# Optimization experiments

Hardware: AMD Instinct MI355X
Metric: run time of the kernel (lower is better)

Reference implementation:

```python
import jax, jax.numpy as jnp
import numpy as np

EPS_LN = 1e-5

def _ln(x, w, b):
    m = x.mean(-1, keepdims=True)
    v = x.var(-1, keepdims=True)  # biased var, matching torch LayerNorm
    return (x - m) / jnp.sqrt(v + EPS_LN) * w + b


def setup_inputs() -> dict:
    key = jax.random.key(0)
    ks = jax.random.split(key, 20)
    B, N, C = 8, 4096, 256
    def lin_w(k, i, o):
        return (jax.random.normal(k, (i, o), jnp.float32) / np.sqrt(i)).astype(jnp.float32)
    inp = {
        'xyz': jax.random.normal(ks[0], (B, N, 3), jnp.float32),
        'features': jax.random.normal(ks[1], (B, N, C), jnp.float32),
        # geo_mlp: Linear(10,32), LN(32), ReLU, Linear(32,16)
        'g_w1': lin_w(ks[2], 10, 32), 'g_b1': jnp.zeros((32,), jnp.float32),
        'g_lnw': jnp.ones((32,), jnp.float32), 'g_lnb': jnp.zeros((32,), jnp.float32),
        'g_w2': lin_w(ks[3], 32, 16), 'g_b2': jnp.zeros((16,), jnp.float32),
        # edge_pred: Linear(C+16,64), LN(64), ReLU, Linear(64,1), Sigmoid
        'e_w1': lin_w(ks[4], C + 16, 64), 'e_b1': jnp.zeros((64,), jnp.float32),
        'e_lnw': jnp.ones((64,), jnp.float32), 'e_lnb': jnp.zeros((64,), jnp.float32),
        'e_w2': lin_w(ks[5], 64, 1), 'e_b2': jnp.zeros((1,), jnp.float32),
        # edge_refine: Linear(C,C), LN(C), ReLU
        'r_w': lin_w(ks[6], C, C), 'r_b': jnp.zeros((C,), jnp.float32),
        'r_lnw': jnp.ones((C,), jnp.float32), 'r_lnb': jnp.zeros((C,), jnp.float32),
    }
    return inp


def reference(xyz, features, g_w1, g_b1, g_lnw, g_lnb, g_w2, g_b2,
              e_w1, e_b1, e_lnw, e_lnb, e_w2, e_b2, r_w, r_b, r_lnw, r_lnb):
    k = 16
    # KNN: pairwise negative squared distance, top-k largest = nearest
    sq = jnp.sum(xyz * xyz, axis=-1)                              # [B,N]
    pd = 2.0 * jnp.einsum('bnd,bmd->bnm', xyz, xyz) - sq[:, :, None] - sq[:, None, :]
    idx = jax.lax.top_k(pd, k)[1]                                 # [B,N,k]
    nbr = jax.vmap(lambda p, i: p[i])(xyz, idx)                   # [B,N,k,3]
    cen = nbr - nbr.mean(axis=2, keepdims=True)                   # centered neighborhoods
    cov = jnp.einsum('bnkc,bnkd->bncd', cen, cen) / k             # [B,N,3,3]
    trace = cov[..., 0, 0] + cov[..., 1, 1] + cov[..., 2, 2]
    det = jnp.clip(cov[..., 0, 0] * cov[..., 1, 1] * cov[..., 2, 2], 1e-8, None)
    std = jnp.std(cen, axis=2, ddof=1)                            # [B,N,3] (torch unbiased std)
    d = jnp.linalg.norm(cen, axis=3)                              # [B,N,k]
    mean_d = d.mean(axis=2)
    std_d = jnp.std(d, axis=2, ddof=1)
    t = trace + 1e-6
    geo = jnp.stack([trace, det, std[..., 0], std[..., 1], std[..., 2],
                     mean_d, std_d, std[..., 0] / t, std[..., 1] / t, std[..., 2] / t], axis=-1)
    geo = jax.nn.relu(_ln(geo @ g_w1 + g_b1, g_lnw, g_lnb)) @ g_w2 + g_b2    # [B,N,16]
    comb = jnp.concatenate([features, geo], axis=-1)
    edge_prob = jax.nn.sigmoid(jax.nn.relu(_ln(comb @ e_w1 + e_b1, e_lnw, e_lnb)) @ e_w2 + e_b2)
    refined = jax.nn.relu(_ln(features @ r_w + r_b, r_lnw, r_lnb))
    refined = features + refined * edge_prob
    return refined, edge_prob
```

## Files before the change

### kernel.cpp

```cpp
#include <hip/hip_runtime.h>
#include <math.h>

#define BATCH 8
#define NPTS  4096
#define CF    256
#define TOPK  16
#define TOTQ  (BATCH*NPTS)
#define EPOFF ((size_t)TOTQ*CF)

typedef __attribute__((ext_vector_type(8))) short bf16x8;
typedef __attribute__((ext_vector_type(4))) float f32x4;

__device__ __forceinline__ unsigned short f2bf(float x) {
    union { float f; unsigned u; } a; a.f = x;
    unsigned r = a.u + 0x7fffu + ((a.u >> 16) & 1u);
    return (unsigned short)(r >> 16);
}
__device__ __forceinline__ float bf2f(unsigned short h) {
    union { float f; unsigned u; } a; a.u = ((unsigned)h) << 16; return a.f;
}
__device__ __forceinline__ void gl_lds16(const void* g, void* l) {
    __builtin_amdgcn_global_load_lds(
        (const __attribute__((address_space(1))) unsigned int*)g,
        (__attribute__((address_space(3))) unsigned int*)l, 16, 0, 0);
}

__global__ __launch_bounds__(256) void prep_k(
    const float* __restrict__ xyz, float4* __restrict__ tab,
    const float* __restrict__ rw, const float* __restrict__ ew1,
    unsigned short* __restrict__ rwh, unsigned short* __restrict__ rwl,
    unsigned short* __restrict__ ewh, unsigned short* __restrict__ ewl)
{
    int t = blockIdx.x*256 + threadIdx.x;
    if (t < TOTQ) {
        float x = xyz[3*t], y = xyz[3*t+1], z = xyz[3*t+2];
        tab[t] = make_float4(x, y, z, x*x + y*y + z*z);
    }
    if (t < 65536) {
        int k = t >> 8, n = t & 255;
        float x = rw[t];
        unsigned short h = f2bf(x);
        unsigned short l = f2bf(x - bf2f(h));
        int dst = (((k>>5)*16 + (n>>4)) << 9) + ((k>>3)&3)*128 + (n&15)*8 + (k&7);
        rwh[dst] = h; rwl[dst] = l;
    }
    if (t < 288*64) {
        int k = t >> 6, n = t & 63;
        float x = (k < 272) ? ew1[k*64 + n] : 0.f;
        unsigned short h = f2bf(x);
        unsigned short l = f2bf(x - bf2f(h));
        int dst = (((k>>5)*4 + (n>>4)) << 9) + ((k>>3)&3)*128 + (n&15)*8 + (k&7);
        ewh[dst] = h; ewl[dst] = l;
    }
}

__global__ __launch_bounds__(512, 4) void knn_geo_k(
    const float4* __restrict__ tab,
    const float* __restrict__ g_w1, const float* __restrict__ g_b1,
    const float* __restrict__ g_lnw, const float* __restrict__ g_lnb,
    const float* __restrict__ g_w2, const float* __restrict__ g_b2,
    float* __restrict__ geo_out)
{
    __shared__ float2 lstS[8][512];
    __shared__ float2 M1[16][64];
    __shared__ float4 coords[64][TOPK+1];
    __shared__ float s_w1[320], s_b1[32], s_lnw[32], s_lnb[32], s_w2[512], s_b2[16];

    const int tid = threadIdx.x;
    if (tid < 320) s_w1[tid] = g_w1[tid];
    s_w2[tid & 511] = g_w2[tid & 511];
    if (tid < 32) { s_b1[tid] = g_b1[tid]; s_lnw[tid] = g_lnw[tid]; s_lnb[tid] = g_lnb[tid]; }
    if (tid < 16) s_b2[tid] = g_b2[tid];

    const int ql = tid & 63;
    const int qg = blockIdx.x*64 + ql;
    const int wv = tid >> 6;
    const int b  = blockIdx.x >> 6;
    const float4* __restrict__ ctab = tab + b*NPTS;
    const int ibase = __builtin_amdgcn_readfirstlane(wv << 9);

    float4 q4 = tab[qg];
    const float qx = q4.x, qy = q4.y, qz = q4.z, qs = q4.w;

    float vals[TOPK]; int idxs[TOPK];
    #pragma unroll
    for (int j = 0; j < TOPK; ++j) { vals[j] = -INFINITY; idxs[j] = 0; }
    int   cnt = 0;
    float thr = -INFINITY;

    auto flushbuf = [&]() {
        for (int e = 0; e < cnt; ++e) {
            float2 en = lstS[e][tid];
            float pv = en.x;
            int   pj = __float_as_int(en.y);
            if (pv > vals[TOPK-1]) {
                #pragma unroll
                for (int j = TOPK-1; j >= 1; --j) {
                    bool ca = pv > vals[j];
                    bool cb = pv > vals[j-1];
                    float t = fminf(pv, vals[j-1]);
                    vals[j] = fmaxf(vals[j], t);
                    int ish = cb ? idxs[j-1] : pj;
                    idxs[j] = ca ? ish : idxs[j];
                }
                bool c0 = pv > vals[0];
                idxs[0] = c0 ? pj : idxs[0];
                vals[0] = fmaxf(vals[0], pv);
            }
        }
    };

    #define EVALC(c, gi)                                                     \
        {                                                                    \
            float dot = fmaf(qx, (c).x, fmaf(qy, (c).y, qz*(c).z));          \
            float pd  = fmaf(2.f, dot, -(qs + (c).w));                       \
            if (pd > thr) {                                                  \
                lstS[cnt][tid] = make_float2(pd, __int_as_float(gi));        \
                ++cnt;                                                       \
            }                                                                \
        }

    {
        const float4* cptr = ctab + ibase;
        float4 A0 = cptr[0], A1 = cptr[1], A2 = cptr[2], A3 = cptr[3];
        for (int ib = 0; ib < 512; ib += 8) {
            float4 B0 = cptr[ib+4], B1 = cptr[ib+5], B2 = cptr[ib+6], B3 = cptr[ib+7];
            EVALC(A0, ibase+ib+0); EVALC(A1, ibase+ib+1);
            EVALC(A2, ibase+ib+2); EVALC(A3, ibase+ib+3);
            if (__any(cnt > 4)) { flushbuf(); cnt = 0; thr = vals[TOPK-1]; }
            A0 = cptr[ib+8]; A1 = cptr[ib+9]; A2 = cptr[ib+10]; A3 = cptr[ib+11];
            EVALC(B0, ibase+ib+4); EVALC(B1, ibase+ib+5);
            EVALC(B2, ibase+ib+6); EVALC(B3, ibase+ib+7);
            if (__any(cnt > 4)) { flushbuf(); cnt = 0; thr = vals[TOPK-1]; }
        }
        flushbuf();
    }
    #undef EVALC

    float2 (*lstP)[256] = (float2(*)[256])&lstS[0][0];

    __syncthreads();
    if (wv < 4) {
        #pragma unroll
        for (int e = 0; e < TOPK; ++e)
            lstP[e][wv*64 + ql] = make_float2(vals[e], __int_as_float(idxs[e]));
    }
    __syncthreads();
    if (tid < 64) {
        const int q = tid;
        int p0 = 0, p1 = 0, p2 = 0, p3 = 0;
        for (int r = 0; r < TOPK; ++r) {
            float2 h0 = lstP[p0][q];
            float2 h1 = lstP[p1][64 + q];
            float2 h2 = lstP[p2][128 + q];
            float2 h3 = lstP[p3][192 + q];
            float best = h0.x; int bj = __float_as_int(h0.y); int bs = 0;
            if (h1.x > best) { best = h1.x; bj = __float_as_int(h1.y); bs = 1; }
            if (h2.x > best) { best = h2.x; bj = __float_as_int(h2.y); bs = 2; }
            if (h3.x > best) { best = h3.x; bj = __float_as_int(h3.y); bs = 3; }
            p0 += (bs == 0); p1 += (bs == 1); p2 += (bs == 2); p3 += (bs == 3);
            M1[r][q] = make_float2(best, __int_as_float(bj));
        }
    }
    __syncthreads();
    if (wv >= 4) {
        #pragma unroll
        for (int e = 0; e < TOPK; ++e)
            lstP[e][(wv-4)*64 + ql] = make_float2(vals[e], __int_as_float(idxs[e]));
    }
    __syncthreads();

    if (tid < 64) {
        const int q = tid;
        int pm = 0, p4 = 0, p5 = 0, p6 = 0, p7 = 0;
        float sx = 0, sy = 0, sz = 0;
        for (int r = 0; r < TOPK; ++r) {
            float2 hm = M1[pm][q];
            float2 h4 = lstP[p4][q];
            float2 h5 = lstP[p5][64 + q];
            float2 h6 = lstP[p6][128 + q];
            float2 h7 = lstP[p7][192 + q];
            float best = hm.x; int bj = __float_as_int(hm.y); int bs = 0;
            if (h4.x > best) { best = h4.x; bj = __float_as_int(h4.y); bs = 1; }
            if (h5.x > best) { best = h5.x; bj = __float_as_int(h5.y); bs = 2; }
            if (h6.x > best) { best = h6.x; bj = __float_as_int(h6.y); bs = 3; }
            if (h7.x > best) { best = h7.x; bj = __float_as_int(h7.y); bs = 4; }
            pm += (bs == 0); p4 += (bs == 1); p5 += (bs == 2); p6 += (bs == 3); p7 += (bs == 4);
            float4 nb = ctab[bj];
            coords[q][r] = nb;
            sx += nb.x; sy += nb.y; sz += nb.z;
        }
        const float mx = sx/16.f, my = sy/16.f, mz = sz/16.f;
        float sxx = 0, syy = 0, szz = 0, sd = 0;
        float dist[TOPK];
        #pragma unroll
        for (int r = 0; r < TOPK; ++r) {
            float4 nb = coords[q][r];
            float cx = nb.x - mx, cy = nb.y - my, cz = nb.z - mz;
            sxx += cx*cx; syy += cy*cy; szz += cz*cz;
            float dd = sqrtf(cx*cx + cy*cy + cz*cz);
            dist[r] = dd; sd += dd;
        }
        const float md = sd/16.f;
        float sdd = 0;
        #pragma unroll
        for (int r = 0; r < TOPK; ++r) { float t = dist[r] - md; sdd += t*t; }
        const float c00 = sxx/16.f, c11 = syy/16.f, c22 = szz/16.f;
        const float trace = c00 + c11 + c22;
        const float det = fmaxf(c00*c11*c22, 1e-8f);
        const float s0 = sqrtf(sxx/15.f), s1 = sqrtf(syy/15.f), s2 = sqrtf(szz/15.f);
        const float stdd = sqrtf(sdd/15.f);
        const float tt = trace + 1e-6f;
        float geo[10] = {trace, det, s0, s1, s2, md, stdd, s0/tt, s1/tt, s2/tt};

        float z1[32];
        #pragma unroll
        for (int jj = 0; jj < 32; ++jj) {
            float a = s_b1[jj];
            #pragma unroll
            for (int i = 0; i < 10; ++i) a = fmaf(geo[i], s_w1[i*32 + jj], a);
            z1[jj] = a;
        }
        float mzn = 0;
        #pragma unroll
        for (int jj = 0; jj < 32; ++jj) mzn += z1[jj];
        mzn /= 32.f;
        float vz = 0;
        #pragma unroll
        for (int jj = 0; jj < 32; ++jj) { float t = z1[jj] - mzn; vz += t*t; }
        vz /= 32.f;
        const float rs = 1.f/sqrtf(vz + 1e-5f);
        #pragma unroll
        for (int jj = 0; jj < 32; ++jj)
            z1[jj] = fmaxf((z1[jj]-mzn)*rs*s_lnw[jj] + s_lnb[jj], 0.f);
        float og[16];
        #pragma unroll
        for (int c = 0; c < 16; ++c) {
            float a = s_b2[c];
            #pragma unroll
            for (int i = 0; i < 32; ++i) a = fmaf(z1[i], s_w2[i*16 + c], a);
            og[c] = a;
        }
        float4* gout = (float4*)(geo_out + (size_t)qg*16);
        gout[0] = make_float4(og[0],  og[1],  og[2],  og[3]);
        gout[1] = make_float4(og[4],  og[5],  og[6],  og[7]);
        gout[2] = make_float4(og[8],  og[9],  og[10], og[11]);
        gout[3] = make_float4(og[12], og[13], og[14], og[15]);
    }
}

__global__ __launch_bounds__(256, 1) void edge_k(
    const float* __restrict__ feat, const float* __restrict__ geo16,
    const unsigned short* __restrict__ rwh, const unsigned short* __restrict__ rwl,
    const unsigned short* __restrict__ ewh, const unsigned short* __restrict__ ewl,
    const float* __restrict__ e_b1, const float* __restrict__ e_lnw,
    const float* __restrict__ e_lnb, const float* __restrict__ e_w2,
    const float* __restrict__ e_b2,
    const float* __restrict__ r_b, const float* __restrict__ r_lnw,
    const float* __restrict__ r_lnb,
    float* __restrict__ out)
{
    __shared__ unsigned short sAh[64*296];
    __shared__ unsigned short sAl[64*296];
    __shared__ unsigned char  sB[65536];
    __shared__ float s_eb1[64], s_elnw[64], s_elnb[64], s_ew2[64];
    __shared__ float s_rb[256], s_rlnw[256], s_rlnb[256];
    __shared__ float s_ep[64], s_m[64], s_rs[64];
    __shared__ float sPx[256], sPq[256];

    const int tid  = threadIdx.x;
    const int lane = tid & 63;
    const int wv   = tid >> 6;
    const int lr   = lane & 15;
    const int lg   = lane >> 4;
    const int pbase = blockIdx.x * 64;

    if (tid < 64) { s_eb1[tid]=e_b1[tid]; s_elnw[tid]=e_lnw[tid]; s_elnb[tid]=e_lnb[tid]; s_ew2[tid]=e_w2[tid]; }
    s_rb[tid]=r_b[tid]; s_rlnw[tid]=r_lnw[tid]; s_rlnb[tid]=r_lnb[tid];

    const float4* f4 = (const float4*)(feat + (size_t)pbase*CF);
    #pragma unroll
    for (int it = 0; it < 16; ++it) {
        int v = tid + it*256;
        float4 x = f4[v];
        int row = v >> 6, c0 = (v & 63)*4;
        unsigned short h0=f2bf(x.x), h1=f2bf(x.y), h2=f2bf(x.z), h3=f2bf(x.w);
        unsigned short l0=f2bf(x.x-bf2f(h0)), l1=f2bf(x.y-bf2f(h1));
        unsigned short l2=f2bf(x.z-bf2f(h2)), l3=f2bf(x.w-bf2f(h3));
        *(ushort4*)&sAh[row*296 + c0] = make_ushort4(h0,h1,h2,h3);
        *(ushort4*)&sAl[row*296 + c0] = make_ushort4(l0,l1,l2,l3);
    }
    {
        const float4* g4 = (const float4*)(geo16 + (size_t)pbase*16);
        float4 x = g4[tid];
        int row = tid >> 2, c0 = 256 + (tid & 3)*4;
        unsigned short h0=f2bf(x.x), h1=f2bf(x.y), h2=f2bf(x.z), h3=f2bf(x.w);
        unsigned short l0=f2bf(x.x-bf2f(h0)), l1=f2bf(x.y-bf2f(h1));
        unsigned short l2=f2bf(x.z-bf2f(h2)), l3=f2bf(x.w-bf2f(h3));
        *(ushort4*)&sAh[row*296 + c0] = make_ushort4(h0,h1,h2,h3);
        *(ushort4*)&sAl[row*296 + c0] = make_ushort4(l0,l1,l2,l3);
        int zc = 272 + (tid & 3)*4;
        *(ushort4*)&sAh[row*296 + zc] = make_ushort4(0,0,0,0);
        *(ushort4*)&sAl[row*296 + zc] = make_ushort4(0,0,0,0);
    }

    auto stage3 = [&](int c, int buf) {
        const char* sh = (const char*)rwh + c*16384;
        const char* sl = (const char*)rwl + c*16384;
        char* dh = (char*)sB + buf*32768;
        char* dl = dh + 16384;
        #pragma unroll
        for (int i = 0; i < 4; ++i) {
            gl_lds16(sh + i*4096 + wv*1024 + lane*16, dh + i*4096 + wv*1024);
            gl_lds16(sl + i*4096 + wv*1024 + lane*16, dl + i*4096 + wv*1024);
        }
    };
    auto stage2 = [&](int c, int buf) {
        const char* sh = (const char*)ewh + c*4096;
        const char* sl = (const char*)ewl + c*4096;
        char* d = (char*)sB + 32768 + buf*8192;
        gl_lds16(sh + wv*1024 + lane*16, d + wv*1024);
        gl_lds16(sl + wv*1024 + lane*16, d + 4096 + wv*1024);
    };

    stage2(0, 0);
    stage3(0, 0);
    __syncthreads();

    f32x4 acc2[4];
    #pragma unroll
    for (int i = 0; i < 4; ++i) acc2[i] = (f32x4){0.f,0.f,0.f,0.f};
    const int arow2 = (wv*16 + lr)*296;
    for (int c = 0; c < 9; ++c) {
        if (c < 8) stage2(c+1, (c+1)&1);
        bf16x8 ah = *(const bf16x8*)&sAh[arow2 + c*32 + lg*8];
        bf16x8 al = *(const bf16x8*)&sAl[arow2 + c*32 + lg*8];
        const unsigned short* bb = (const unsigned short*)(sB + 32768 + (c&1)*8192);
        #pragma unroll
        for (int nt = 0; nt < 4; ++nt) {
            bf16x8 bh = *(const bf16x8*)&bb[nt*512 + lane*8];
            bf16x8 bl = *(const bf16x8*)&bb[2048 + nt*512 + lane*8];
            acc2[nt] = __builtin_amdgcn_mfma_f32_16x16x32_bf16(al, bh, acc2[nt], 0,0,0);
            acc2[nt] = __builtin_amdgcn_mfma_f32_16x16x32_bf16(ah, bl, acc2[nt], 0,0,0);
            acc2[nt] = __builtin_amdgcn_mfma_f32_16x16x32_bf16(ah, bh, acc2[nt], 0,0,0);
        }
        __syncthreads();
    }

    {
        float px[4] = {0,0,0,0}, pq[4] = {0,0,0,0};
        #pragma unroll
        for (int nt = 0; nt < 4; ++nt) {
            float bv = s_eb1[nt*16 + lr];
            #pragma unroll
            for (int j = 0; j < 4; ++j) {
                acc2[nt][j] += bv;
                px[j] += acc2[nt][j];
                pq[j] += acc2[nt][j]*acc2[nt][j];
            }
        }
        #pragma unroll
        for (int sw = 1; sw < 16; sw <<= 1) {
            #pragma unroll
            for (int j = 0; j < 4; ++j) { px[j] += __shfl_xor(px[j], sw); pq[j] += __shfl_xor(pq[j], sw); }
        }
        float mj[4], rj[4], dd[4] = {0,0,0,0};
        #pragma unroll
        for (int j = 0; j < 4; ++j) {
            mj[j] = px[j]*(1.f/64.f);
            float var = pq[j]*(1.f/64.f) - mj[j]*mj[j];
            rj[j] = rsqrtf(var + 1e-5f);
        }
        #pragma unroll
        for (int nt = 0; nt < 4; ++nt) {
            int col = nt*16 + lr;
            float lw = s_elnw[col], lb = s_elnb[col], w2 = s_ew2[col];
            #pragma unroll
            for (int j = 0; j < 4; ++j) {
                float h = fmaxf((acc2[nt][j]-mj[j])*rj[j]*lw + lb, 0.f);
                dd[j] = fmaf(h, w2, dd[j]);
            }
        }
        #pragma unroll
        for (int sw = 1; sw < 16; sw <<= 1) {
            #pragma unroll
            for (int j = 0; j < 4; ++j) dd[j] += __shfl_xor(dd[j], sw);
        }
        float eb2v = e_b2[0];
        #pragma unroll
        for (int j = 0; j < 4; ++j) {
            if (lr == j) {
                int row = wv*16 + lg*4 + j;
                float ep = 1.f/(1.f + expf(-(dd[j] + eb2v)));
                s_ep[row] = ep;
                out[EPOFF + pbase + row] = ep;
            }
        }
    }

    f32x4 acc3[4][4];
    #pragma unroll
    for (int mt = 0; mt < 4; ++mt)
        #pragma unroll
        for (int nt = 0; nt < 4; ++nt) acc3[mt][nt] = (f32x4){0.f,0.f,0.f,0.f};

    for (int c = 0; c < 8; ++c) {
        if (c < 7) stage3(c+1, (c+1)&1);
        bf16x8 ah[4], al[4];
        #pragma unroll
        for (int mt = 0; mt < 4; ++mt) {
            ah[mt] = *(const bf16x8*)&sAh[(mt*16+lr)*296 + c*32 + lg*8];
            al[mt] = *(const bf16x8*)&sAl[(mt*16+lr)*296 + c*32 + lg*8];
        }
        const unsigned short* bb = (const unsigned short*)(sB + (c&1)*32768);
        #pragma unroll
        for (int ntl = 0; ntl < 4; ++ntl) {
            int nt = wv*4 + ntl;
            bf16x8 bh = *(const bf16x8*)&bb[nt*512 + lane*8];
            bf16x8 bl = *(const bf16x8*)&bb[8192 + nt*512 + lane*8];
            #pragma unroll
            for (int mt = 0; mt < 4; ++mt) {
                acc3[mt][ntl] = __builtin_amdgcn_mfma_f32_16x16x32_bf16(al[mt], bh, acc3[mt][ntl], 0,0,0);
                acc3[mt][ntl] = __builtin_amdgcn_mfma_f32_16x16x32_bf16(ah[mt], bl, acc3[mt][ntl], 0,0,0);
                acc3[mt][ntl] = __builtin_amdgcn_mfma_f32_16x16x32_bf16(ah[mt], bh, acc3[mt][ntl], 0,0,0);
            }
        }
        __syncthreads();
    }

    float qx[4][4], qq[4][4];
    #pragma unroll
    for (int mt = 0; mt < 4; ++mt)
        #pragma unroll
        for (int j = 0; j < 4; ++j) { qx[mt][j] = 0.f; qq[mt][j] = 0.f; }
    #pragma unroll
    for (int ntl = 0; ntl < 4; ++ntl) {
        int col = (wv*4 + ntl)*16 + lr;
        float bv = s_rb[col];
        #pragma unroll
        for (int mt = 0; mt < 4; ++mt)
            #pragma unroll
            for (int j = 0; j < 4; ++j) {
                acc3[mt][ntl][j] += bv;
                float v = acc3[mt][ntl][j];
                qx[mt][j] += v; qq[mt][j] += v*v;
            }
    }
    #pragma unroll
    for (int sw = 1; sw < 16; sw <<= 1) {
        #pragma unroll
        for (int mt = 0; mt < 4; ++mt)
            #pragma unroll
            for (int j = 0; j < 4; ++j) { qx[mt][j] += __shfl_xor(qx[mt][j], sw); qq[mt][j] += __shfl_xor(qq[mt][j], sw); }
    }
    if (lr == 0) {
        #pragma unroll
        for (int mt = 0; mt < 4; ++mt)
            #pragma unroll
            for (int j = 0; j < 4; ++j) {
                int row = mt*16 + lg*4 + j;
                sPx[wv*64 + row] = qx[mt][j];
                sPq[wv*64 + row] = qq[mt][j];
            }
    }
    __syncthreads();
    if (tid < 64) {
        float Sx = sPx[tid] + sPx[64+tid] + sPx[128+tid] + sPx[192+tid];
        float Sq = sPq[tid] + sPq[64+tid] + sPq[128+tid] + sPq[192+tid];
        float m  = Sx*(1.f/256.f);
        float var = Sq*(1.f/256.f) - m*m;
        s_m[tid]  = m;
        s_rs[tid] = rsqrtf(var + 1e-5f);
    }
    __syncthreads();

    {
        float* sOut = (float*)sB;
        float lwv[4], lbv[4]; int colv[4];
        #pragma unroll
        for (int ntl = 0; ntl < 4; ++ntl) {
            colv[ntl] = (wv*4 + ntl)*16 + lr;
            lwv[ntl] = s_rlnw[colv[ntl]];
            lbv[ntl] = s_rlnb[colv[ntl]];
        }
        #pragma unroll
        for (int mt = 0; mt < 4; ++mt) {
            #pragma unroll
            for (int j = 0; j < 4; ++j) {
                int row = mt*16 + lg*4 + j;
                float m = s_m[row], rs = s_rs[row];
                #pragma unroll
                for (int ntl = 0; ntl < 4; ++ntl) {
                    float h = fmaxf((acc3[mt][ntl][j]-m)*rs*lwv[ntl] + lbv[ntl], 0.f);
                    sOut[row*256 + colv[ntl]] = h;
                }
            }
        }
    }
    __syncthreads();

    {
        const float* sOut = (const float*)sB;
        #pragma unroll
        for (int it = 0; it < 16; ++it) {
            int v = tid + it*256;
            int row = v >> 6, c0 = (v & 63)*4;
            float4 h4 = *(const float4*)&sOut[row*256 + c0];
            ushort4 hh = *(const ushort4*)&sAh[row*296 + c0];
            ushort4 ll = *(const ushort4*)&sAl[row*296 + c0];
            float ep = s_ep[row];
            float4 o;
            o.x = bf2f(hh.x) + bf2f(ll.x) + h4.x*ep;
            o.y = bf2f(hh.y) + bf2f(ll.y) + h4.y*ep;
            o.z = bf2f(hh.z) + bf2f(ll.z) + h4.z*ep;
            o.w = bf2f(hh.w) + bf2f(ll.w) + h4.w*ep;
            *(float4*)&out[(size_t)(pbase+row)*CF + c0] = o;
        }
    }
}

extern "C" void kernel_launch(void* const* d_in, const int* in_sizes, int n_in,
                              void* d_out, int out_size, void* d_ws, size_t ws_size,
                              hipStream_t stream) {
    (void)in_sizes; (void)n_in; (void)out_size; (void)ws_size;
    const float* xyz   = (const float*)d_in[0];
    const float* feat  = (const float*)d_in[1];
    const float* g_w1  = (const float*)d_in[2];
    const float* g_b1  = (const float*)d_in[3];
    const float* g_lnw = (const float*)d_in[4];
    const float* g_lnb = (const float*)d_in[5];
    const float* g_w2  = (const float*)d_in[6];
    const float* g_b2  = (const float*)d_in[7];
    const float* e_w1  = (const float*)d_in[8];
    const float* e_b1  = (const float*)d_in[9];
    const float* e_lnw = (const float*)d_in[10];
    const float* e_lnb = (const float*)d_in[11];
    const float* e_w2  = (const float*)d_in[12];
    const float* e_b2  = (const float*)d_in[13];
    const float* r_w   = (const float*)d_in[14];
    const float* r_b   = (const float*)d_in[15];
    const float* r_lnw = (const float*)d_in[16];
    const float* r_lnb = (const float*)d_in[17];
    float* out = (float*)d_out;

    char* ws = (char*)d_ws;
    float*          geo_ws = (float*)ws;
    float4*         tab    = (float4*)(ws + 0x200000);
    unsigned short* rwh    = (unsigned short*)(ws + 0x280000);
    unsigned short* rwl    = (unsigned short*)(ws + 0x2A0000);
    unsigned short* ewh    = (unsigned short*)(ws + 0x2C0000);
    unsigned short* ewl    = (unsigned short*)(ws + 0x2D0000);

    hipLaunchKernelGGL(prep_k, dim3(256), dim3(256), 0, stream,
                       xyz, tab, r_w, e_w1, rwh, rwl, ewh, ewl);
    hipLaunchKernelGGL(knn_geo_k, dim3(TOTQ/64), dim3(512), 0, stream,
                       tab, g_w1, g_b1, g_lnw, g_lnb, g_w2, g_b2, geo_ws);
    hipLaunchKernelGGL(edge_k, dim3(TOTQ/64), dim3(256), 0, stream,
                       feat, geo_ws, rwh, rwl, ewh, ewl,
                       e_b1, e_lnw, e_lnb, e_w2, e_b2,
                       r_b, r_lnw, r_lnb, out);
}
```

Before: 314.9 us.

## Split KNN scan across 4 waves per block with single-pass merge and cheaper key

Each block now scans candidates with 4 waves of 1024 points each instead of 8 waves of 512, which removes the two-stage merge and the M1 buffer so one 4-way merge runs after a single barrier. The distance key is rescaled to dot minus half the squared norms, with the -0.5 factor folded into the precomputed table, so each candidate costs one fma chain and the ranking is unchanged. The flush threshold rises from more than 4 to more than 12 buffered entries so flushes happen less often, and the loads for the next group are double-buffered. Neighbor coordinates stay in registers instead of LDS, and std_d comes from a one-pass variance formula, which can lose some precision through cancellation. With half the waves per query, each thread does twice as much serial scan work, so latency hiding now depends more on occupancy.

```diff
diff --git a/kernel.cpp b/kernel.cpp
--- a/kernel.cpp
+++ b/kernel.cpp
@@ -34,7 +34,7 @@
     int t = blockIdx.x*256 + threadIdx.x;
     if (t < TOTQ) {
         float x = xyz[3*t], y = xyz[3*t+1], z = xyz[3*t+2];
-        tab[t] = make_float4(x, y, z, x*x + y*y + z*z);
+        tab[t] = make_float4(x, y, z, -0.5f*(x*x + y*y + z*z));
     }
     if (t < 65536) {
         int k = t >> 8, n = t & 255;
@@ -54,21 +54,19 @@
     }
 }
 
-__global__ __launch_bounds__(512, 4) void knn_geo_k(
+__global__ __launch_bounds__(256, 2) void knn_geo_k(
     const float4* __restrict__ tab,
     const float* __restrict__ g_w1, const float* __restrict__ g_b1,
     const float* __restrict__ g_lnw, const float* __restrict__ g_lnb,
     const float* __restrict__ g_w2, const float* __restrict__ g_b2,
     float* __restrict__ geo_out)
 {
-    __shared__ float2 lstS[8][512];
-    __shared__ float2 M1[16][64];
-    __shared__ float4 coords[64][TOPK+1];
+    __shared__ float2 lst[TOPK][256];
     __shared__ float s_w1[320], s_b1[32], s_lnw[32], s_lnb[32], s_w2[512], s_b2[16];
 
     const int tid = threadIdx.x;
-    if (tid < 320) s_w1[tid] = g_w1[tid];
-    s_w2[tid & 511] = g_w2[tid & 511];
+    for (int v = tid; v < 320; v += 256) s_w1[v] = g_w1[v];
+    for (int v = tid; v < 512; v += 256) s_w2[v] = g_w2[v];
     if (tid < 32) { s_b1[tid] = g_b1[tid]; s_lnw[tid] = g_lnw[tid]; s_lnb[tid] = g_lnb[tid]; }
     if (tid < 16) s_b2[tid] = g_b2[tid];
 
@@ -77,10 +75,10 @@
     const int wv = tid >> 6;
     const int b  = blockIdx.x >> 6;
     const float4* __restrict__ ctab = tab + b*NPTS;
-    const int ibase = __builtin_amdgcn_readfirstlane(wv << 9);
+    const int ibase = __builtin_amdgcn_readfirstlane(wv << 10);
 
     float4 q4 = tab[qg];
-    const float qx = q4.x, qy = q4.y, qz = q4.z, qs = q4.w;
+    const float qx = q4.x, qy = q4.y, qz = q4.z, qh = q4.w;
 
     float vals[TOPK]; int idxs[TOPK];
     #pragma unroll
@@ -90,7 +88,7 @@
 
     auto flushbuf = [&]() {
         for (int e = 0; e < cnt; ++e) {
-            float2 en = lstS[e][tid];
+            float2 en = lst[e][tid];
             float pv = en.x;
             int   pj = __float_as_int(en.y);
             if (pv > vals[TOPK-1]) {
@@ -103,8 +101,7 @@
                     int ish = cb ? idxs[j-1] : pj;
                     idxs[j] = ca ? ish : idxs[j];
                 }
-                bool c0 = pv > vals[0];
-                idxs[0] = c0 ? pj : idxs[0];
+                idxs[0] = (pv > vals[0]) ? pj : idxs[0];
                 vals[0] = fmaxf(vals[0], pv);
             }
         }
@@ -112,10 +109,10 @@
 
     #define EVALC(c, gi)                                                     \
         {                                                                    \
-            float dot = fmaf(qx, (c).x, fmaf(qy, (c).y, qz*(c).z));          \
-            float pd  = fmaf(2.f, dot, -(qs + (c).w));                       \
-            if (pd > thr) {                                                  \
-                lstS[cnt][tid] = make_float2(pd, __int_as_float(gi));        \
+            float s0 = (c).w + qh;                                           \
+            float key = fmaf(qx, (c).x, fmaf(qy, (c).y, fmaf(qz, (c).z, s0)));\
+            if (key > thr) {                                                 \
+                lst[cnt][tid] = make_float2(key, __int_as_float(gi));        \
                 ++cnt;                                                       \
             }                                                                \
         }
@@ -123,95 +120,71 @@
     {
         const float4* cptr = ctab + ibase;
         float4 A0 = cptr[0], A1 = cptr[1], A2 = cptr[2], A3 = cptr[3];
-        for (int ib = 0; ib < 512; ib += 8) {
-            float4 B0 = cptr[ib+4], B1 = cptr[ib+5], B2 = cptr[ib+6], B3 = cptr[ib+7];
+        float4 B0 = cptr[4], B1 = cptr[5], B2 = cptr[6], B3 = cptr[7];
+        for (int ib = 0; ib < 1024; ib += 8) {
             EVALC(A0, ibase+ib+0); EVALC(A1, ibase+ib+1);
             EVALC(A2, ibase+ib+2); EVALC(A3, ibase+ib+3);
-            if (__any(cnt > 4)) { flushbuf(); cnt = 0; thr = vals[TOPK-1]; }
-            A0 = cptr[ib+8]; A1 = cptr[ib+9]; A2 = cptr[ib+10]; A3 = cptr[ib+11];
+            if (__any(cnt > 12)) { flushbuf(); cnt = 0; thr = vals[TOPK-1]; }
+            if (ib + 8 < 1024) {
+                A0 = cptr[ib+8]; A1 = cptr[ib+9]; A2 = cptr[ib+10]; A3 = cptr[ib+11];
+            }
             EVALC(B0, ibase+ib+4); EVALC(B1, ibase+ib+5);
             EVALC(B2, ibase+ib+6); EVALC(B3, ibase+ib+7);
-            if (__any(cnt > 4)) { flushbuf(); cnt = 0; thr = vals[TOPK-1]; }
+            if (__any(cnt > 12)) { flushbuf(); cnt = 0; thr = vals[TOPK-1]; }
+            if (ib + 8 < 1024) {
+                B0 = cptr[ib+12]; B1 = cptr[ib+13]; B2 = cptr[ib+14]; B3 = cptr[ib+15];
+            }
         }
         flushbuf();
     }
     #undef EVALC
 
-    float2 (*lstP)[256] = (float2(*)[256])&lstS[0][0];
-
     __syncthreads();
-    if (wv < 4) {
-        #pragma unroll
-        for (int e = 0; e < TOPK; ++e)
-            lstP[e][wv*64 + ql] = make_float2(vals[e], __int_as_float(idxs[e]));
-    }
+    #pragma unroll
+    for (int e = 0; e < TOPK; ++e)
+        lst[e][tid] = make_float2(vals[e], __int_as_float(idxs[e]));
     __syncthreads();
+
     if (tid < 64) {
         const int q = tid;
         int p0 = 0, p1 = 0, p2 = 0, p3 = 0;
+        float nbx[TOPK], nby[TOPK], nbz[TOPK];
+        float sx = 0, sy = 0, sz = 0;
+        #pragma unroll
         for (int r = 0; r < TOPK; ++r) {
-            float2 h0 = lstP[p0][q];
-            float2 h1 = lstP[p1][64 + q];
-            float2 h2 = lstP[p2][128 + q];
-            float2 h3 = lstP[p3][192 + q];
+            float2 h0 = lst[p0][q];
+            float2 h1 = lst[p1][64 + q];
+            float2 h2 = lst[p2][128 + q];
+            float2 h3 = lst[p3][192 + q];
             float best = h0.x; int bj = __float_as_int(h0.y); int bs = 0;
             if (h1.x > best) { best = h1.x; bj = __float_as_int(h1.y); bs = 1; }
             if (h2.x > best) { best = h2.x; bj = __float_as_int(h2.y); bs = 2; }
             if (h3.x > best) { best = h3.x; bj = __float_as_int(h3.y); bs = 3; }
             p0 += (bs == 0); p1 += (bs == 1); p2 += (bs == 2); p3 += (bs == 3);
-            M1[r][q] = make_float2(best, __int_as_float(bj));
-        }
-    }
-    __syncthreads();
-    if (wv >= 4) {
-        #pragma unroll
-        for (int e = 0; e < TOPK; ++e)
-            lstP[e][(wv-4)*64 + ql] = make_float2(vals[e], __int_as_float(idxs[e]));
-    }
-    __syncthreads();
-
-    if (tid < 64) {
-        const int q = tid;
-        int pm = 0, p4 = 0, p5 = 0, p6 = 0, p7 = 0;
-        float sx = 0, sy = 0, sz = 0;
-        for (int r = 0; r < TOPK; ++r) {
-            float2 hm = M1[pm][q];
-            float2 h4 = lstP[p4][q];
-            float2 h5 = lstP[p5][64 + q];
-            float2 h6 = lstP[p6][128 + q];
-            float2 h7 = lstP[p7][192 + q];
-            float best = hm.x; int bj = __float_as_int(hm.y); int bs = 0;
-            if (h4.x > best) { best = h4.x; bj = __float_as_int(h4.y); bs = 1; }
-            if (h5.x > best) { best = h5.x; bj = __float_as_int(h5.y); bs = 2; }
-            if (h6.x > best) { best = h6.x; bj = __float_as_int(h6.y); bs = 3; }
-            if (h7.x > best) { best = h7.x; bj = __float_as_int(h7.y); bs = 4; }
-            pm += (bs == 0); p4 += (bs == 1); p5 += (bs == 2); p6 += (bs == 3); p7 += (bs == 4);
             float4 nb = ctab[bj];
-            coords[q][r] = nb;
+            nbx[r] = nb.x; nby[r] = nb.y; nbz[r] = nb.z;
             sx += nb.x; sy += nb.y; sz += nb.z;
         }
         const float mx = sx/16.f, my = sy/16.f, mz = sz/16.f;
         float sxx = 0, syy = 0, szz = 0, sd = 0;
-        float dist[TOPK];
         #pragma unroll
         for (int r = 0; r < TOPK; ++r) {
-            float4 nb = coords[q][r];
-            float cx = nb.x - mx, cy = nb.y - my, cz = nb.z - mz;
-            sxx += cx*cx; syy += cy*cy; szz += cz*cz;
-            float dd = sqrtf(cx*cx + cy*cy + cz*cz);
-            dist[r] = dd; sd += dd;
-        }
-        const float md = sd/16.f;
-        float sdd = 0;
-        #pragma unroll
-        for (int r = 0; r < TOPK; ++r) { float t = dist[r] - md; sdd += t*t; }
+            float cx = nbx[r] - mx, cy = nby[r] - my, cz = nbz[r] - mz;
+            float xx = cx*cx, yy = cy*cy, zz = cz*cz;
+            sxx += xx; syy += yy; szz += zz;
+            sd += sqrtf(xx + yy + zz);
+        }
+        const float md  = sd * (1.f/16.f);
+        const float sd2 = sxx + syy + szz;
+        const float sdd = fmaxf(sd2 - sd*sd*(1.f/16.f), 0.f);
         const float c00 = sxx/16.f, c11 = syy/16.f, c22 = szz/16.f;
         const float trace = c00 + c11 + c22;
         const float det = fmaxf(c00*c11*c22, 1e-8f);
         const float s0 = sqrtf(sxx/15.f), s1 = sqrtf(syy/15.f), s2 = sqrtf(szz/15.f);
         const float stdd = sqrtf(sdd/15.f);
         const float tt = trace + 1e-6f;
-        float geo[10] = {trace, det, s0, s1, s2, md, stdd, s0/tt, s1/tt, s2/tt};
+        const float rt = 1.f/tt;
+        float geo[10] = {trace, det, s0, s1, s2, md, stdd, s0*rt, s1*rt, s2*rt};
 
         float z1[32];
         #pragma unroll
@@ -553,7 +526,7 @@
 
     hipLaunchKernelGGL(prep_k, dim3(256), dim3(256), 0, stream,
                        xyz, tab, r_w, e_w1, rwh, rwl, ewh, ewl);
-    hipLaunchKernelGGL(knn_geo_k, dim3(TOTQ/64), dim3(512), 0, stream,
+    hipLaunchKernelGGL(knn_geo_k, dim3(TOTQ/64), dim3(256), 0, stream,
                        tab, g_w1, g_b1, g_lnw, g_lnb, g_w2, g_b2, geo_ws);
     hipLaunchKernelGGL(edge_k, dim3(TOTQ/64), dim3(256), 0, stream,
                        feat, geo_ws, rwh, rwl, ewh, ewl,
```

New measurement: 322.7 us. +2.5%, slower.
